# Performance work log

Measured on AMD Instinct MI355X. Metric: run time of the kernel, lower is better.

The kernel has to match this reference:

```python
import jax, jax.numpy as jnp
import numpy as np

L, B, H, IN = 4, 256, 1024, 1024

def setup_inputs() -> dict:
    key = jax.random.key(0)
    ks = jax.random.split(key, 7)
    return {
        "x": jax.random.normal(ks[0], (B, IN), jnp.float32),
        "h0": jax.random.normal(ks[1], (L, B, H), jnp.float32),
        "c0": jax.random.normal(ks[2], (L, B, H), jnp.float32),
        "w_ih": jax.random.normal(ks[3], (L, 4 * H, IN), jnp.float32) * 0.02,
        "w_hh": jax.random.normal(ks[4], (L, 4 * H, H), jnp.float32) * 0.02,
        "b_ih": jax.random.normal(ks[5], (L, 4 * H), jnp.float32) * 0.02,
        "b_hh": jax.random.normal(ks[6], (L, 4 * H), jnp.float32) * 0.02,
    }

def _lstm_cell(inp, h, c, wi, wh, bi, bh):
    # gates: (B, 4H), PyTorch gate order i, f, g, o
    gates = jnp.dot(inp, wi.T) + jnp.dot(h, wh.T) + bi + bh
    i_g, f_g, g_g, o_g = jnp.split(gates, 4, axis=-1)
    c_new = jax.nn.sigmoid(f_g) * c + jax.nn.sigmoid(i_g) * jnp.tanh(g_g)
    h_new = jax.nn.sigmoid(o_g) * jnp.tanh(c_new)
    return h_new, c_new

def reference(x, h0, c0, w_ih, w_hh, b_ih, b_hh):
    # Sequential over layers (inter-layer dependency); dropout is identity (eval mode / p=0).
    inp = x
    hs, cs = [], []
    for i in range(h0.shape[0]):
        h, c = _lstm_cell(inp, h0[i], c0[i], w_ih[i], w_hh[i], b_ih[i], b_hh[i])
        hs.append(h)
        cs.append(c)
        inp = h
    return jnp.stack(hs, axis=0), jnp.stack(cs, axis=0)
```

## Files before the change

kernel.cpp:

```cpp
#include <hip/hip_runtime.h>

#define NLAYER 4
#define BATCH  256
#define HID    1024

typedef float f32x4 __attribute__((ext_vector_type(4)));
typedef short short8 __attribute__((ext_vector_type(8)));

#define BARRIER() __asm__ __volatile__("s_waitcnt lgkmcnt(0)\ns_barrier" ::: "memory")

__device__ __forceinline__ unsigned short f2bf(float f) {
  unsigned int u = __float_as_uint(f);
  unsigned int r = u + 0x7fffu + ((u >> 16) & 1u);
  return (unsigned short)(r >> 16);
}
__device__ __forceinline__ float sigm(float x) { return 1.f / (1.f + __expf(-x)); }
__device__ __forceinline__ float tanh_(float x) { return 2.f / (1.f + __expf(-2.f * x)) - 1.f; }

__global__ __launch_bounds__(512, 2) void lstm_fused(
    const float* __restrict__ A0, const float* __restrict__ A1,
    const float* __restrict__ W0, const float* __restrict__ W1,
    const float* __restrict__ bi, const float* __restrict__ bh,
    const float* __restrict__ c0l,
    float* __restrict__ hout, float* __restrict__ cout) {
  __shared__ union U {
    unsigned short stage[2][2][64 * 72];
    float sg[4 * 64 * 17];
  } sm;
  __shared__ float bsum[64];

  const int tid  = threadIdx.x;
  const int h0c  = blockIdx.x * 16;
  const int m0   = blockIdx.y * 64;
  const int lane = tid & 63;
  const int w    = tid >> 6;
  const int wm   = w & 3;
  const int wn   = w >> 1 & 0;
  const int wcol = w >> 2;
  const int lrow = lane & 15, lq = lane >> 4;
  (void)wn;

  if (tid < 64) {
    int g = tid >> 4, hc = tid & 15;
    bsum[tid] = bi[g * 1024 + h0c + hc] + bh[g * 1024 + h0c + hc];
  }

  const int r0  = tid >> 4;
  const int kk0 = (tid & 15) << 2;
  const int wr0 = (r0 >> 4) * 1024 + h0c + (r0 & 15);
  const int r1  = r0 + 32;
  const int wr1 = (r1 >> 4) * 1024 + h0c + (r1 & 15);

  float4 ra[2], rb[2];
  auto loadAB = [&](int kt) {
    const float* ab; const float* wb; int col;
    if (kt < 16) { ab = A0; wb = W0; col = kt * 64; }
    else         { ab = A1; wb = W1; col = (kt - 16) * 64; }
    ra[0] = *reinterpret_cast<const float4*>(ab + (size_t)(m0 + r0) * 1024 + col + kk0);
    ra[1] = *reinterpret_cast<const float4*>(ab + (size_t)(m0 + r1) * 1024 + col + kk0);
    rb[0] = *reinterpret_cast<const float4*>(wb + (size_t)wr0 * 1024 + col + kk0);
    rb[1] = *reinterpret_cast<const float4*>(wb + (size_t)wr1 * 1024 + col + kk0);
  };

  f32x4 acc[2];
  acc[0] = (f32x4){0.f, 0.f, 0.f, 0.f};
  acc[1] = (f32x4){0.f, 0.f, 0.f, 0.f};

  loadAB(0);
  for (int kt = 0; kt < 32; ++kt) {
    const int buf = kt & 1;
#pragma unroll
    for (int i = 0; i < 2; ++i) {
      int r = r0 + (i << 5);
      ushort4 pa, pb;
      pa.x = f2bf(ra[i].x); pa.y = f2bf(ra[i].y); pa.z = f2bf(ra[i].z); pa.w = f2bf(ra[i].w);
      pb.x = f2bf(rb[i].x); pb.y = f2bf(rb[i].y); pb.z = f2bf(rb[i].z); pb.w = f2bf(rb[i].w);
      *reinterpret_cast<ushort4*>(&sm.stage[buf][0][r * 72 + kk0]) = pa;
      *reinterpret_cast<ushort4*>(&sm.stage[buf][1][r * 72 + kk0]) = pb;
    }
    if (kt < 31) loadAB(kt + 1);
    BARRIER();
#pragma unroll
    for (int kk = 0; kk < 64; kk += 32) {
      short8 af  = *reinterpret_cast<const short8*>(
          &sm.stage[buf][0][(wm * 16 + lrow) * 72 + kk + lq * 8]);
      short8 bf0 = *reinterpret_cast<const short8*>(
          &sm.stage[buf][1][(wcol * 32 + lrow) * 72 + kk + lq * 8]);
      short8 bf1 = *reinterpret_cast<const short8*>(
          &sm.stage[buf][1][(wcol * 32 + 16 + lrow) * 72 + kk + lq * 8]);
      acc[0] = __builtin_amdgcn_mfma_f32_16x16x32_bf16(af, bf0, acc[0], 0, 0, 0);
      acc[1] = __builtin_amdgcn_mfma_f32_16x16x32_bf16(af, bf1, acc[1], 0, 0, 0);
    }
  }

  BARRIER();

#pragma unroll
  for (int nt = 0; nt < 2; ++nt) {
    int gate = wcol * 2 + nt;
    int rowb = wm * 16 + lq * 4;
#pragma unroll
    for (int r = 0; r < 4; ++r)
      sm.sg[gate * 1088 + (rowb + r) * 17 + lrow] = acc[nt][r];
  }
  BARRIER();

  {
    int row = tid >> 3;
    int hp  = (tid & 7) * 2;
    float2 cp = *reinterpret_cast<const float2*>(c0l + (size_t)(m0 + row) * 1024 + h0c + hp);
    float cpa[2] = {cp.x, cp.y};
    float hva[2], cva[2];
#pragma unroll
    for (int e = 0; e < 2; ++e) {
      int hc = hp + e;
      float gi = sm.sg[0 * 1088 + row * 17 + hc] + bsum[0  + hc];
      float gf = sm.sg[1 * 1088 + row * 17 + hc] + bsum[16 + hc];
      float gg = sm.sg[2 * 1088 + row * 17 + hc] + bsum[32 + hc];
      float go = sm.sg[3 * 1088 + row * 17 + hc] + bsum[48 + hc];
      float cn = sigm(gf) * cpa[e] + sigm(gi) * tanh_(gg);
      cva[e] = cn;
      hva[e] = sigm(go) * tanh_(cn);
    }
    float2 hv; hv.x = hva[0]; hv.y = hva[1];
    float2 cv; cv.x = cva[0]; cv.y = cva[1];
    *reinterpret_cast<float2*>(hout + (size_t)(m0 + row) * 1024 + h0c + hp) = hv;
    *reinterpret_cast<float2*>(cout + (size_t)(m0 + row) * 1024 + h0c + hp) = cv;
  }
}

extern "C" void kernel_launch(void* const* d_in, const int* in_sizes, int n_in,
                              void* d_out, int out_size, void* d_ws, size_t ws_size,
                              hipStream_t stream) {
  const float* x    = (const float*)d_in[0];
  const float* h0   = (const float*)d_in[1];
  const float* c0   = (const float*)d_in[2];
  const float* w_ih = (const float*)d_in[3];
  const float* w_hh = (const float*)d_in[4];
  const float* b_ih = (const float*)d_in[5];
  const float* b_hh = (const float*)d_in[6];
  float* out = (float*)d_out;

  const size_t BH = (size_t)BATCH * HID;
  const size_t WL = (size_t)4 * HID * HID;

  for (int l = 0; l < NLAYER; ++l) {
    const float* A0 = (l == 0) ? x : out + (size_t)(l - 1) * BH;
    lstm_fused<<<dim3(64, 4), 512, 0, stream>>>(
        A0, h0 + (size_t)l * BH,
        w_ih + (size_t)l * WL, w_hh + (size_t)l * WL,
        b_ih + (size_t)l * 4096, b_hh + (size_t)l * 4096,
        c0 + (size_t)l * BH,
        out + (size_t)l * BH, out + (size_t)NLAYER * BH + (size_t)l * BH);
  }
}
```

Before: 264.1 us.

## Deepen global prefetch to three stages and XOR-swizzle LDS tiles

Global loads are now prefetched three k-tiles ahead into a four-slot register ring instead of one tile ahead, which hides more memory latency in this bandwidth-bound GEMM. The LDS staging tiles drop their padding and use an XOR swizzle to avoid bank conflicts. The c0 load is hoisted to the kernel start so it overlaps the main loop. The deeper ring raises register pressure, which may hurt occupancy under launch_bounds(512,2).

```diff
diff --git a/kernel.cpp b/kernel.cpp
--- a/kernel.cpp
+++ b/kernel.cpp
@@ -17,6 +17,13 @@
 __device__ __forceinline__ float sigm(float x) { return 1.f / (1.f + __expf(-x)); }
 __device__ __forceinline__ float tanh_(float x) { return 2.f / (1.f + __expf(-2.f * x)) - 1.f; }
 
+__device__ __forceinline__ int lds_w(int r, int kk0) {
+  return r * 64 + (((kk0 >> 3) ^ (r & 7)) << 3) + (kk0 & 7);
+}
+__device__ __forceinline__ int lds_r(int row, int c) {
+  return row * 64 + ((c ^ (row & 7)) << 3);
+}
+
 __global__ __launch_bounds__(512, 2) void lstm_fused(
     const float* __restrict__ A0, const float* __restrict__ A1,
     const float* __restrict__ W0, const float* __restrict__ W1,
@@ -24,7 +31,7 @@
     const float* __restrict__ c0l,
     float* __restrict__ hout, float* __restrict__ cout) {
   __shared__ union U {
-    unsigned short stage[2][2][64 * 72];
+    unsigned short stage[2][2][64 * 64];
     float sg[4 * 64 * 17];
   } sm;
   __shared__ float bsum[64];
@@ -35,10 +42,8 @@
   const int lane = tid & 63;
   const int w    = tid >> 6;
   const int wm   = w & 3;
-  const int wn   = w >> 1 & 0;
   const int wcol = w >> 2;
   const int lrow = lane & 15, lq = lane >> 4;
-  (void)wn;
 
   if (tid < 64) {
     int g = tid >> 4, hc = tid & 15;
@@ -48,48 +53,63 @@
   const int r0  = tid >> 4;
   const int kk0 = (tid & 15) << 2;
   const int wr0 = (r0 >> 4) * 1024 + h0c + (r0 & 15);
-  const int r1  = r0 + 32;
-  const int wr1 = (r1 >> 4) * 1024 + h0c + (r1 & 15);
 
-  float4 ra[2], rb[2];
-  auto loadAB = [&](int kt) {
-    const float* ab; const float* wb; int col;
-    if (kt < 16) { ab = A0; wb = W0; col = kt * 64; }
-    else         { ab = A1; wb = W1; col = (kt - 16) * 64; }
-    ra[0] = *reinterpret_cast<const float4*>(ab + (size_t)(m0 + r0) * 1024 + col + kk0);
-    ra[1] = *reinterpret_cast<const float4*>(ab + (size_t)(m0 + r1) * 1024 + col + kk0);
-    rb[0] = *reinterpret_cast<const float4*>(wb + (size_t)wr0 * 1024 + col + kk0);
-    rb[1] = *reinterpret_cast<const float4*>(wb + (size_t)wr1 * 1024 + col + kk0);
+  const float* pA0 = A0 + (size_t)(m0 + r0) * 1024 + kk0;
+  const float* pA1 = A1 + (size_t)(m0 + r0) * 1024 + kk0;
+  const float* pW0 = W0 + (size_t)wr0 * 1024 + kk0;
+  const float* pW1 = W1 + (size_t)wr0 * 1024 + kk0;
+
+  const int erow = tid >> 3;
+  const int ehp  = (tid & 7) * 2;
+  float2 cp = *reinterpret_cast<const float2*>(
+      c0l + (size_t)(m0 + erow) * 1024 + h0c + ehp);
+
+  float4 ra[4][2], rb[4][2];
+  auto loadAB = [&](int kt, int s) {
+    const float* pa = (kt < 16 ? pA0 : pA1) + (kt & 15) * 64;
+    const float* pb = (kt < 16 ? pW0 : pW1) + (kt & 15) * 64;
+    ra[s][0] = *reinterpret_cast<const float4*>(pa);
+    ra[s][1] = *reinterpret_cast<const float4*>(pa + 32 * 1024);
+    rb[s][0] = *reinterpret_cast<const float4*>(pb);
+    rb[s][1] = *reinterpret_cast<const float4*>(pb + 2048 * 1024);
   };
 
   f32x4 acc[2];
   acc[0] = (f32x4){0.f, 0.f, 0.f, 0.f};
   acc[1] = (f32x4){0.f, 0.f, 0.f, 0.f};
 
-  loadAB(0);
-  for (int kt = 0; kt < 32; ++kt) {
-    const int buf = kt & 1;
+  loadAB(0, 0); loadAB(1, 1); loadAB(2, 2);
+
+  for (int kt4 = 0; kt4 < 32; kt4 += 4) {
 #pragma unroll
-    for (int i = 0; i < 2; ++i) {
-      int r = r0 + (i << 5);
-      ushort4 pa, pb;
-      pa.x = f2bf(ra[i].x); pa.y = f2bf(ra[i].y); pa.z = f2bf(ra[i].z); pa.w = f2bf(ra[i].w);
-      pb.x = f2bf(rb[i].x); pb.y = f2bf(rb[i].y); pb.z = f2bf(rb[i].z); pb.w = f2bf(rb[i].w);
-      *reinterpret_cast<ushort4*>(&sm.stage[buf][0][r * 72 + kk0]) = pa;
-      *reinterpret_cast<ushort4*>(&sm.stage[buf][1][r * 72 + kk0]) = pb;
-    }
-    if (kt < 31) loadAB(kt + 1);
-    BARRIER();
+    for (int ks = 0; ks < 4; ++ks) {
+      const int kt  = kt4 + ks;
+      const int buf = ks & 1;
 #pragma unroll
-    for (int kk = 0; kk < 64; kk += 32) {
-      short8 af  = *reinterpret_cast<const short8*>(
-          &sm.stage[buf][0][(wm * 16 + lrow) * 72 + kk + lq * 8]);
-      short8 bf0 = *reinterpret_cast<const short8*>(
-          &sm.stage[buf][1][(wcol * 32 + lrow) * 72 + kk + lq * 8]);
-      short8 bf1 = *reinterpret_cast<const short8*>(
-          &sm.stage[buf][1][(wcol * 32 + 16 + lrow) * 72 + kk + lq * 8]);
-      acc[0] = __builtin_amdgcn_mfma_f32_16x16x32_bf16(af, bf0, acc[0], 0, 0, 0);
-      acc[1] = __builtin_amdgcn_mfma_f32_16x16x32_bf16(af, bf1, acc[1], 0, 0, 0);
+      for (int i = 0; i < 2; ++i) {
+        int r = r0 + (i << 5);
+        ushort4 pa, pb;
+        pa.x = f2bf(ra[ks][i].x); pa.y = f2bf(ra[ks][i].y);
+        pa.z = f2bf(ra[ks][i].z); pa.w = f2bf(ra[ks][i].w);
+        pb.x = f2bf(rb[ks][i].x); pb.y = f2bf(rb[ks][i].y);
+        pb.z = f2bf(rb[ks][i].z); pb.w = f2bf(rb[ks][i].w);
+        *reinterpret_cast<ushort4*>(&sm.stage[buf][0][lds_w(r, kk0)]) = pa;
+        *reinterpret_cast<ushort4*>(&sm.stage[buf][1][lds_w(r, kk0)]) = pb;
+      }
+      if (kt < 29) loadAB(kt + 3, (ks + 3) & 3);
+      BARRIER();
+#pragma unroll
+      for (int kk = 0; kk < 64; kk += 32) {
+        const int cb = kk >> 3;
+        short8 af = *reinterpret_cast<const short8*>(
+            &sm.stage[buf][0][lds_r(wm * 16 + lrow, cb + lq)]);
+        short8 bf0 = *reinterpret_cast<const short8*>(
+            &sm.stage[buf][1][lds_r(wcol * 32 + lrow, cb + lq)]);
+        short8 bf1 = *reinterpret_cast<const short8*>(
+            &sm.stage[buf][1][lds_r(wcol * 32 + 16 + lrow, cb + lq)]);
+        acc[0] = __builtin_amdgcn_mfma_f32_16x16x32_bf16(af, bf0, acc[0], 0, 0, 0);
+        acc[1] = __builtin_amdgcn_mfma_f32_16x16x32_bf16(af, bf1, acc[1], 0, 0, 0);
+      }
     }
   }
 
@@ -106,26 +126,23 @@
   BARRIER();
 
   {
-    int row = tid >> 3;
-    int hp  = (tid & 7) * 2;
-    float2 cp = *reinterpret_cast<const float2*>(c0l + (size_t)(m0 + row) * 1024 + h0c + hp);
     float cpa[2] = {cp.x, cp.y};
     float hva[2], cva[2];
 #pragma unroll
     for (int e = 0; e < 2; ++e) {
-      int hc = hp + e;
-      float gi = sm.sg[0 * 1088 + row * 17 + hc] + bsum[0  + hc];
-      float gf = sm.sg[1 * 1088 + row * 17 + hc] + bsum[16 + hc];
-      float gg = sm.sg[2 * 1088 + row * 17 + hc] + bsum[32 + hc];
-      float go = sm.sg[3 * 1088 + row * 17 + hc] + bsum[48 + hc];
+      int hc = ehp + e;
+      float gi = sm.sg[0 * 1088 + erow * 17 + hc] + bsum[0  + hc];
+      float gf = sm.sg[1 * 1088 + erow * 17 + hc] + bsum[16 + hc];
+      float gg = sm.sg[2 * 1088 + erow * 17 + hc] + bsum[32 + hc];
+      float go = sm.sg[3 * 1088 + erow * 17 + hc] + bsum[48 + hc];
       float cn = sigm(gf) * cpa[e] + sigm(gi) * tanh_(gg);
       cva[e] = cn;
       hva[e] = sigm(go) * tanh_(cn);
     }
     float2 hv; hv.x = hva[0]; hv.y = hva[1];
     float2 cv; cv.x = cva[0]; cv.y = cva[1];
-    *reinterpret_cast<float2*>(hout + (size_t)(m0 + row) * 1024 + h0c + hp) = hv;
-    *reinterpret_cast<float2*>(cout + (size_t)(m0 + row) * 1024 + h0c + hp) = cv;
+    *reinterpret_cast<float2*>(hout + (size_t)(m0 + erow) * 1024 + h0c + ehp) = hv;
+    *reinterpret_cast<float2*>(cout + (size_t)(m0 + erow) * 1024 + h0c + ehp) = cv;
   }
 }
 
```

Result: no change. 263.6 us (-0.2%).
